# Kernel tuning notes

Hardware: AMD Instinct MI355X
Metric: run time of the kernel (lower is better)

Reference implementation:

```python
import jax, jax.numpy as jnp
import numpy as np

D = 1024      # total input features
R = 32        # number of ragged regions
RMAX = 32     # max region size (padding target)
HIDDEN = [128, 128]
H1, H2 = HIDDEN
B = 8192      # batch size


def _made_masks(r, rmax, hidden):
    """TFP AutoregressiveNetwork masks (left-to-right order, 'equal' hidden degrees,
    params=2, use_bias=False), zero-padded to rmax features."""
    order = np.arange(1, r + 1)
    degs = [order]
    for u in hidden:
        mn = min(int(degs[-1].min()), r - 1)
        degs.append(np.maximum(mn, np.ceil(np.arange(1, u + 1) * (r - 1) / float(u + 1)).astype(np.int64)))
    m1 = np.zeros((rmax, hidden[0]), bool)
    m1[:r] = degs[0][:, None] <= degs[1][None, :]
    m2 = degs[1][:, None] <= degs[2][None, :]
    mout = np.zeros((hidden[-1], rmax * 2), bool)
    out_deg = np.repeat(order, 2)  # output layout is feature-major: [feat, param]
    mout[:, :2 * r] = degs[-1][:, None] < out_deg[None, :]
    return m1, m2, mout


def setup_inputs() -> dict:
    rng = np.random.default_rng(0)
    perm = rng.permutation(D)
    sizes = rng.integers(8, RMAX + 1, size=R)
    idx = np.zeros((R, RMAX), np.int64)
    valid = np.zeros((R, RMAX), bool)
    M1 = np.zeros((R, RMAX, H1), bool)
    M2 = np.zeros((R, H1, H2), bool)
    Mout = np.zeros((R, H2, RMAX * 2), bool)
    pos = 0
    for i in range(R):
        s = int(sizes[i])
        idx[i, :s] = perm[pos:pos + s]
        pos += s
        valid[i, :s] = True
        M1[i], M2[i], Mout[i] = _made_masks(s, RMAX, HIDDEN)
    key = jax.random.key(0)
    k1, k2, k3, k4 = jax.random.split(key, 4)
    inputs = jax.random.normal(k1, (B, D), jnp.float32)
    W1 = jax.random.normal(k2, (R, RMAX, H1), jnp.float32) / np.float32(np.sqrt(RMAX))
    W2 = jax.random.normal(k3, (R, H1, H2), jnp.float32) / np.float32(np.sqrt(H1))
    Wout = jax.random.normal(k4, (R, H2, RMAX * 2), jnp.float32) / np.float32(np.sqrt(H2))
    return {"inputs": inputs, "W1": W1, "W2": W2, "Wout": Wout,
            "idx": jnp.asarray(idx), "valid": jnp.asarray(valid),
            "M1": jnp.asarray(M1), "M2": jnp.asarray(M2), "Mout": jnp.asarray(Mout)}


def reference(inputs, W1, W2, Wout, idx, valid, M1, M2, Mout):
    f = inputs.dtype
    v = valid.astype(f)                              # [R, RMAX]
    xg = jnp.take(inputs, idx, axis=1) * v           # [B, R, RMAX] ragged gather (padded)
    # MADE masked MLP (relu, no bias), batched over all regions at once
    h1 = jax.nn.relu(jnp.einsum('brd,rdh->brh', xg, W1 * M1.astype(f)))
    h2 = jax.nn.relu(jnp.einsum('brh,rhk->brk', h1, W2 * M2.astype(f)))
    out = jnp.einsum('brk,rko->bro', h2, Wout * Mout.astype(f))
    out = out.reshape(out.shape[0], out.shape[1], RMAX, 2)
    shift, log_s = out[..., 0], out[..., 1]
    # MAF inverse: u = (x - shift) * exp(-log_scale); logdet = -sum(log_scale)
    u = (xg - shift) * jnp.exp(-log_s)
    elem = -0.5 * u * u - 0.5 * jnp.log(2.0 * jnp.pi) - log_s
    ll = jnp.sum(elem * v, axis=-1)                  # [B, R]
    return ll[..., None]                             # [B, R, 1] as in tf.stack of expand_dims
```

## Files before the change

kernel.cpp:

```cpp
#include <hip/hip_runtime.h>
#include <math.h>


#define RR 32
#define DD 1024
#define HH 128
#define OO 64
#define TROWS 64
#define TILES 8
#define BLOCKS_PER_R 16

#define SHP 136
#define SXG 40
#define SSC 136

typedef _Float16 f16x8_t __attribute__((ext_vector_type(8)));
typedef float f32x4_t __attribute__((ext_vector_type(4)));
typedef unsigned short u16;
typedef unsigned int u32;

__device__ __forceinline__ u32 pkrtz(float a, float b) {
    union { __fp16 v __attribute__((ext_vector_type(2))); u32 u; } c;
    c.v = __builtin_amdgcn_cvt_pkrtz(a, b);
    return c.u;
}
__device__ __forceinline__ f32x4_t mfma16h(f16x8_t a, f16x8_t b, f32x4_t c) {
    return __builtin_amdgcn_mfma_f32_16x16x32_f16(a, b, c, 0, 0, 0);
}

__device__ __forceinline__ void stage_block16(const float* __restrict__ W,
                                              const int* __restrict__ M,
                                              int ldc, int c0, int K, u16* dst,
                                              int tid)
{
    const int kb = tid >> 3;
    const int cb = tid & 7;
    if (kb * 4 >= K) return;
    const int k0 = kb * 4;
    float e[4][4];
#pragma unroll
    for (int i = 0; i < 4; ++i) {
        const int o = ((k0 + i) * ldc + c0 + 4 * cb) >> 2;
        float4 w = ((const float4*)W)[o];
        int4   m = ((const int4*)M)[o];
        e[i][0] = m.x ? w.x : 0.f; e[i][1] = m.y ? w.y : 0.f;
        e[i][2] = m.z ? w.z : 0.f; e[i][3] = m.w ? w.w : 0.f;
    }
#pragma unroll
    for (int j = 0; j < 4; ++j) {
        uint2 p;
        p.x = pkrtz(e[0][j], e[1][j]);
        p.y = pkrtz(e[2][j], e[3][j]);
        *(uint2*)&dst[(4 * cb + j) * SSC + k0] = p;
    }
}

__device__ __forceinline__ void relu_store16(u16* __restrict__ dst, int o, f32x4_t a)
{
    uint2 s;
    s.x = pkrtz(fmaxf(a[0], 0.f), fmaxf(a[1], 0.f));
    s.y = pkrtz(fmaxf(a[2], 0.f), fmaxf(a[3], 0.f));
    *(uint2*)&dst[o] = s;
}

__global__ __launch_bounds__(512, 4)
void made_flow_r24(const float* __restrict__ inputs,
                   const float* __restrict__ W1,
                   const float* __restrict__ W2,
                   const float* __restrict__ Wout,
                   const int* __restrict__ idx,
                   const int* __restrict__ valid,
                   const int* __restrict__ M1,
                   const int* __restrict__ M2,
                   const int* __restrict__ Mout,
                   float* __restrict__ out)
{
    __shared__ __align__(16) u16 h1s[TROWS * SHP];
    __shared__ __align__(16) u16 h2s[TROWS * SHP];
    __shared__ __align__(16) u16 wout_lds[OO * SSC];
    __shared__ __align__(16) u16 xgh[2][TROWS * SXG];
    __shared__ __align__(16) float red2[2][TROWS][4];
    __shared__ int   idx_s[RR];
    __shared__ float v_s[RR];

    u16* const scr  = h1s;
    u16* const scr2 = h2s;

    const int tid  = threadIdx.x;
    const int r    = blockIdx.x / BLOCKS_PER_R;
    const int rb   = blockIdx.x % BLOCKS_PER_R;
    const int ts64 = rb * TILES * TROWS;

    const int lane = tid & 63;
    const int wave = tid >> 6;
    const int q    = lane >> 4;
    const int l16  = lane & 15;
    const int mq   = wave & 3;
    const int nh   = wave >> 2;
    const int wm3  = wave & 3;
    const int ni3  = wave >> 2;

    if (tid < RR) {
        idx_s[tid] = idx[r * RR + tid];
        v_s[tid]   = valid[r * RR + tid] ? 1.f : 0.f;
    }

    f16x8_t a1[2];
    f16x8_t a2[2][4];
    {
        const float* W1r = W1 + r * RR * HH;   const int* M1r = M1 + r * RR * HH;
        const float* W2r = W2 + r * HH * HH;   const int* M2r = M2 + r * HH * HH;
        const float* Wor = Wout + r * HH * OO; const int* Mor = Mout + r * HH * OO;
        for (int i = 0; i < 2; ++i) {
            __syncthreads();
            if (tid < 256) stage_block16(W2r, M2r, HH, 32 * (2 * i),     HH, scr,  tid);
            else           stage_block16(W2r, M2r, HH, 32 * (2 * i + 1), HH, scr2, tid - 256);
            __syncthreads();
            if (mq == 2 * i) {
#pragma unroll
                for (int mi = 0; mi < 2; ++mi)
#pragma unroll
                    for (int ks = 0; ks < 4; ++ks)
                        a2[mi][ks] = *(const f16x8_t*)&scr[(16 * mi + l16) * SSC + ks * 32 + q * 8];
            } else if (mq == 2 * i + 1) {
#pragma unroll
                for (int mi = 0; mi < 2; ++mi)
#pragma unroll
                    for (int ks = 0; ks < 4; ++ks)
                        a2[mi][ks] = *(const f16x8_t*)&scr2[(16 * mi + l16) * SSC + ks * 32 + q * 8];
            }
        }
        for (int i = 0; i < 2; ++i) {
            __syncthreads();
            if (tid < 256) stage_block16(W1r, M1r, HH, 32 * (2 * i),     RR, scr,  tid);
            else           stage_block16(W1r, M1r, HH, 32 * (2 * i + 1), RR, scr2, tid - 256);
            __syncthreads();
            if (mq == 2 * i) {
#pragma unroll
                for (int mi = 0; mi < 2; ++mi)
                    a1[mi] = *(const f16x8_t*)&scr [(16 * mi + l16) * SSC + q * 8];
            } else if (mq == 2 * i + 1) {
#pragma unroll
                for (int mi = 0; mi < 2; ++mi)
                    a1[mi] = *(const f16x8_t*)&scr2[(16 * mi + l16) * SSC + q * 8];
            }
        }
        if (tid < 256) stage_block16(Wor, Mor, OO, 0,  HH, wout_lds,            tid);
        else           stage_block16(Wor, Mor, OO, 32, HH, wout_lds + 32 * SSC, tid - 256);
    }
    __syncthreads();

    const f32x4_t zero4 = {0.f, 0.f, 0.f, 0.f};
    const int grow = tid >> 4;
    const int gg   = tid & 15;
    const int   ci0 = idx_s[2 * gg], ci1 = idx_s[2 * gg + 1];
    const float cv0 = v_s[2 * gg],   cv1 = v_s[2 * gg + 1];
    const int j0  = 8 * wm3 + 2 * q;
    const float vj0 = v_s[j0], vj1 = v_s[j0 + 1];
    const int gb0 = (ts64 + grow) * DD;
    const int gb1 = (ts64 + 32 + grow) * DD;

    float gx[4];
    {
        float a0 = inputs[gb0 + ci0] * cv0, a1v = inputs[gb0 + ci1] * cv1;
        float b0 = inputs[gb1 + ci0] * cv0, b1v = inputs[gb1 + ci1] * cv1;
        *(u32*)&xgh[0][grow * SXG + 2 * gg]        = pkrtz(a0, a1v);
        *(u32*)&xgh[0][(grow + 32) * SXG + 2 * gg] = pkrtz(b0, b1v);
        gx[0] = inputs[gb0 + TROWS * DD + ci0] * cv0;
        gx[1] = inputs[gb0 + TROWS * DD + ci1] * cv1;
        gx[2] = inputs[gb1 + TROWS * DD + ci0] * cv0;
        gx[3] = inputs[gb1 + TROWS * DD + ci1] * cv1;
    }
    __syncthreads();

    {
#pragma unroll
        for (int nn = 0; nn < 2; ++nn) {
            const int rw = 16 * (2 * nh + nn) + l16;
            f16x8_t b = *(const f16x8_t*)&xgh[0][rw * SXG + q * 8];
#pragma unroll
            for (int mi = 0; mi < 2; ++mi) {
                f32x4_t a = mfma16h(a1[mi], b, zero4);
                relu_store16(h1s, rw * SHP + 32 * mq + 16 * mi + 4 * q, a);
            }
        }
    }

    for (int t = 0; t < TILES; ++t) {
        __syncthreads();

        const bool dg = (t + 1 < TILES);

        if (dg) {
            *(u32*)&xgh[(t + 1) & 1][grow * SXG + 2 * gg]        = pkrtz(gx[0], gx[1]);
            *(u32*)&xgh[(t + 1) & 1][(grow + 32) * SXG + 2 * gg] = pkrtz(gx[2], gx[3]);
        }
        {
            f32x4_t acc[2][2] = {{zero4, zero4}, {zero4, zero4}};
            __builtin_amdgcn_s_setprio(1);
#pragma unroll
            for (int ks = 0; ks < 4; ++ks) {
#pragma unroll
                for (int nn = 0; nn < 2; ++nn) {
                    f16x8_t b = *(const f16x8_t*)&h1s[(16 * (2 * nh + nn) + l16) * SHP + ks * 32 + q * 8];
#pragma unroll
                    for (int mi = 0; mi < 2; ++mi)
                        acc[mi][nn] = mfma16h(a2[mi][ks], b, acc[mi][nn]);
                }
            }
            __builtin_amdgcn_s_setprio(0);
#pragma unroll
            for (int mi = 0; mi < 2; ++mi)
#pragma unroll
                for (int nn = 0; nn < 2; ++nn)
                    relu_store16(h2s, (16 * (2 * nh + nn) + l16) * SHP + 32 * mq + 16 * mi + 4 * q,
                                 acc[mi][nn]);
        }
        if (t >= 2 && tid < TROWS) {
            float4 rv = *(const float4*)&red2[t & 1][tid][0];
            out[((rb * TILES + (t - 2)) * TROWS + tid) * RR + r] =
                rv.x + rv.y + rv.z + rv.w;
        }
        __syncthreads();

        if (t + 2 < TILES) {
            const int base = (t + 2) * (TROWS * DD);
            gx[0] = inputs[gb0 + base + ci0] * cv0;
            gx[1] = inputs[gb0 + base + ci1] * cv1;
            gx[2] = inputs[gb1 + base + ci0] * cv0;
            gx[3] = inputs[gb1 + base + ci1] * cv1;
        }

        f32x4_t acc3[2] = {zero4, zero4};
        __builtin_amdgcn_s_setprio(1);
#pragma unroll
        for (int ks = 0; ks < 4; ++ks) {
            f16x8_t ao = *(const f16x8_t*)&wout_lds[(16 * wm3 + l16) * SSC + ks * 32 + q * 8];
#pragma unroll
            for (int nn = 0; nn < 2; ++nn) {
                f16x8_t b = *(const f16x8_t*)&h2s[(16 * (ni3 + 2 * nn) + l16) * SHP + ks * 32 + q * 8];
                acc3[nn] = mfma16h(ao, b, acc3[nn]);
            }
        }
        __builtin_amdgcn_s_setprio(0);

        if (dg) {
#pragma unroll
            for (int nn = 0; nn < 2; ++nn) {
                const int rw = 16 * (2 * nh + nn) + l16;
                f16x8_t b = *(const f16x8_t*)&xgh[(t + 1) & 1][rw * SXG + q * 8];
#pragma unroll
                for (int mi = 0; mi < 2; ++mi) {
                    f32x4_t a = mfma16h(a1[mi], b, zero4);
                    relu_store16(h1s, rw * SHP + 32 * mq + 16 * mi + 4 * q, a);
                }
            }
        }

#pragma unroll
        for (int nn = 0; nn < 2; ++nn) {
            const int row = 16 * (ni3 + 2 * nn) + l16;
            u32 xw = *(const u32*)&xgh[t & 1][row * SXG + j0];
            union { u32 u; _Float16 h[2]; } xc; xc.u = xw;
            const float xv0 = (float)xc.h[0], xv1 = (float)xc.h[1];
            f32x4_t a = acc3[nn];
            const float u0 = (xv0 - a[0]) * __expf(-a[1]);
            const float u1 = (xv1 - a[2]) * __expf(-a[3]);
            float p = (-0.5f * u0 * u0 - 0.91893853320467266954f - a[1]) * vj0
                    + (-0.5f * u1 * u1 - 0.91893853320467266954f - a[3]) * vj1;
            p += __shfl_xor(p, 16, 64);
            p += __shfl_xor(p, 32, 64);
            if (q == 0) red2[t & 1][row][wm3] = p;
        }
    }

    __syncthreads();
    if (tid < 2 * TROWS) {
        const int tt  = TILES - 2 + (tid >> 6);
        const int row = tid & 63;
        float4 rv = *(const float4*)&red2[tt & 1][row][0];
        out[((rb * TILES + tt) * TROWS + row) * RR + r] =
            rv.x + rv.y + rv.z + rv.w;
    }
}

extern "C" void kernel_launch(void* const* d_in, const int* in_sizes, int n_in,
                              void* d_out, int out_size, void* d_ws, size_t ws_size,
                              hipStream_t stream)
{
    const float* inputs = (const float*)d_in[0];
    const float* W1     = (const float*)d_in[1];
    const float* W2     = (const float*)d_in[2];
    const float* Wout   = (const float*)d_in[3];
    const int*   idx    = (const int*)d_in[4];
    const int*   valid  = (const int*)d_in[5];
    const int*   M1     = (const int*)d_in[6];
    const int*   M2     = (const int*)d_in[7];
    const int*   Mout   = (const int*)d_in[8];
    float*       out    = (float*)d_out;

    hipLaunchKernelGGL(made_flow_r24, dim3(RR * BLOCKS_PER_R), dim3(512), 0, stream,
                       inputs, W1, W2, Wout, idx, valid, M1, M2, Mout, out);
}
```

Before: 117.1 us.

## Halve tile rows and block size, keep Wout fragments in registers

Blocks shrink from 512 to 256 threads with 32-row tiles, and the grid doubles to 32 blocks per region, so each region's rows are spread over more, smaller blocks. Each wave now owns a 32-column slice of every layer, and the Wout fragments are held in registers instead of being reread from a dedicated LDS buffer each tile. This removes the wout_lds array and its per-tile LDS reads and raises block-level parallelism. The cost is that every block redoes the masked-weight staging, so that prologue work doubles overall, and register pressure rises.

```diff
diff --git a/kernel.cpp b/kernel.cpp
--- a/kernel.cpp
+++ b/kernel.cpp
@@ -6,13 +6,14 @@
 #define DD 1024
 #define HH 128
 #define OO 64
-#define TROWS 64
+#define TROWS 32
 #define TILES 8
-#define BLOCKS_PER_R 16
+#define BLOCKS_PER_R 32
 
 #define SHP 136
 #define SXG 40
 #define SSC 136
+#define SW1 40
 
 typedef _Float16 f16x8_t __attribute__((ext_vector_type(8)));
 typedef float f32x4_t __attribute__((ext_vector_type(4)));
@@ -30,8 +31,8 @@
 
 __device__ __forceinline__ void stage_block16(const float* __restrict__ W,
                                               const int* __restrict__ M,
-                                              int ldc, int c0, int K, u16* dst,
-                                              int tid)
+                                              int ldc, int c0, int K,
+                                              u16* dst, int sd, int tid)
 {
     const int kb = tid >> 3;
     const int cb = tid & 7;
@@ -51,7 +52,7 @@
         uint2 p;
         p.x = pkrtz(e[0][j], e[1][j]);
         p.y = pkrtz(e[2][j], e[3][j]);
-        *(uint2*)&dst[(4 * cb + j) * SSC + k0] = p;
+        *(uint2*)&dst[(4 * cb + j) * sd + k0] = p;
     }
 }
 
@@ -63,8 +64,8 @@
     *(uint2*)&dst[o] = s;
 }
 
-__global__ __launch_bounds__(512, 4)
-void made_flow_r24(const float* __restrict__ inputs,
+__global__ __launch_bounds__(256, 4)
+void made_flow_r25(const float* __restrict__ inputs,
                    const float* __restrict__ W1,
                    const float* __restrict__ W2,
                    const float* __restrict__ Wout,
@@ -77,7 +78,6 @@
 {
     __shared__ __align__(16) u16 h1s[TROWS * SHP];
     __shared__ __align__(16) u16 h2s[TROWS * SHP];
-    __shared__ __align__(16) u16 wout_lds[OO * SSC];
     __shared__ __align__(16) u16 xgh[2][TROWS * SXG];
     __shared__ __align__(16) float red2[2][TROWS][4];
     __shared__ int   idx_s[RR];
@@ -89,16 +89,13 @@
     const int tid  = threadIdx.x;
     const int r    = blockIdx.x / BLOCKS_PER_R;
     const int rb   = blockIdx.x % BLOCKS_PER_R;
-    const int ts64 = rb * TILES * TROWS;
+    const int ts   = rb * TILES;
 
     const int lane = tid & 63;
     const int wave = tid >> 6;
     const int q    = lane >> 4;
     const int l16  = lane & 15;
-    const int mq   = wave & 3;
-    const int nh   = wave >> 2;
-    const int wm3  = wave & 3;
-    const int ni3  = wave >> 2;
+    const int mq   = wave;
 
     if (tid < RR) {
         idx_s[tid] = idx[r * RR + tid];
@@ -107,76 +104,81 @@
 
     f16x8_t a1[2];
     f16x8_t a2[2][4];
+    f16x8_t ao[4];
     {
         const float* W1r = W1 + r * RR * HH;   const int* M1r = M1 + r * RR * HH;
         const float* W2r = W2 + r * HH * HH;   const int* M2r = M2 + r * HH * HH;
         const float* Wor = Wout + r * HH * OO; const int* Mor = Mout + r * HH * OO;
-        for (int i = 0; i < 2; ++i) {
+        for (int c = 0; c < 4; ++c) {
             __syncthreads();
-            if (tid < 256) stage_block16(W2r, M2r, HH, 32 * (2 * i),     HH, scr,  tid);
-            else           stage_block16(W2r, M2r, HH, 32 * (2 * i + 1), HH, scr2, tid - 256);
+            stage_block16(W2r, M2r, HH, 32 * c, HH, scr, SSC, tid);
             __syncthreads();
-            if (mq == 2 * i) {
+            if (mq == c) {
 #pragma unroll
                 for (int mi = 0; mi < 2; ++mi)
 #pragma unroll
                     for (int ks = 0; ks < 4; ++ks)
                         a2[mi][ks] = *(const f16x8_t*)&scr[(16 * mi + l16) * SSC + ks * 32 + q * 8];
-            } else if (mq == 2 * i + 1) {
-#pragma unroll
-                for (int mi = 0; mi < 2; ++mi)
-#pragma unroll
-                    for (int ks = 0; ks < 4; ++ks)
-                        a2[mi][ks] = *(const f16x8_t*)&scr2[(16 * mi + l16) * SSC + ks * 32 + q * 8];
-            }
-        }
-        for (int i = 0; i < 2; ++i) {
+            }
+        }
+        for (int c = 0; c < 2; ++c) {
             __syncthreads();
-            if (tid < 256) stage_block16(W1r, M1r, HH, 32 * (2 * i),     RR, scr,  tid);
-            else           stage_block16(W1r, M1r, HH, 32 * (2 * i + 1), RR, scr2, tid - 256);
+            stage_block16(Wor, Mor, OO, 32 * c, HH, scr, SSC, tid);
             __syncthreads();
-            if (mq == 2 * i) {
-#pragma unroll
-                for (int mi = 0; mi < 2; ++mi)
-                    a1[mi] = *(const f16x8_t*)&scr [(16 * mi + l16) * SSC + q * 8];
-            } else if (mq == 2 * i + 1) {
-#pragma unroll
-                for (int mi = 0; mi < 2; ++mi)
-                    a1[mi] = *(const f16x8_t*)&scr2[(16 * mi + l16) * SSC + q * 8];
-            }
-        }
-        if (tid < 256) stage_block16(Wor, Mor, OO, 0,  HH, wout_lds,            tid);
-        else           stage_block16(Wor, Mor, OO, 32, HH, wout_lds + 32 * SSC, tid - 256);
+            if ((wave >> 1) == c) {
+#pragma unroll
+                for (int ks = 0; ks < 4; ++ks)
+                    ao[ks] = *(const f16x8_t*)&scr[(16 * (wave & 1) + l16) * SSC + ks * 32 + q * 8];
+            }
+        }
+        __syncthreads();
+        {
+            const int c  = tid >> 6;
+            const int tp = tid & 63;
+            u16* dst = (c < 2 ? scr : scr2) + 32 * (c & 1) * SW1;
+            stage_block16(W1r, M1r, HH, 32 * c, RR, dst, SW1, tp);
+        }
+        __syncthreads();
+        {
+            const u16* s = (mq < 2) ? scr : scr2;
+#pragma unroll
+            for (int mi = 0; mi < 2; ++mi)
+                a1[mi] = *(const f16x8_t*)&s[(32 * (mq & 1) + 16 * mi + l16) * SW1 + q * 8];
+        }
     }
     __syncthreads();
 
     const f32x4_t zero4 = {0.f, 0.f, 0.f, 0.f};
-    const int grow = tid >> 4;
-    const int gg   = tid & 15;
-    const int   ci0 = idx_s[2 * gg], ci1 = idx_s[2 * gg + 1];
-    const float cv0 = v_s[2 * gg],   cv1 = v_s[2 * gg + 1];
-    const int j0  = 8 * wm3 + 2 * q;
+    const int grow = tid >> 3;
+    const int gg   = tid & 7;
+    int   ci[4]; float cv[4];
+#pragma unroll
+    for (int u = 0; u < 4; ++u) {
+        ci[u] = idx_s[4 * gg + u];
+        cv[u] = v_s[4 * gg + u];
+    }
+    const int j0  = 8 * mq + 2 * q;
     const float vj0 = v_s[j0], vj1 = v_s[j0 + 1];
-    const int gb0 = (ts64 + grow) * DD;
-    const int gb1 = (ts64 + 32 + grow) * DD;
+    const int gbase = (ts * TROWS + grow) * DD;
 
     float gx[4];
     {
-        float a0 = inputs[gb0 + ci0] * cv0, a1v = inputs[gb0 + ci1] * cv1;
-        float b0 = inputs[gb1 + ci0] * cv0, b1v = inputs[gb1 + ci1] * cv1;
-        *(u32*)&xgh[0][grow * SXG + 2 * gg]        = pkrtz(a0, a1v);
-        *(u32*)&xgh[0][(grow + 32) * SXG + 2 * gg] = pkrtz(b0, b1v);
-        gx[0] = inputs[gb0 + TROWS * DD + ci0] * cv0;
-        gx[1] = inputs[gb0 + TROWS * DD + ci1] * cv1;
-        gx[2] = inputs[gb1 + TROWS * DD + ci0] * cv0;
-        gx[3] = inputs[gb1 + TROWS * DD + ci1] * cv1;
+        float a0 = inputs[gbase + ci[0]] * cv[0];
+        float a1v = inputs[gbase + ci[1]] * cv[1];
+        float a2v = inputs[gbase + ci[2]] * cv[2];
+        float a3 = inputs[gbase + ci[3]] * cv[3];
+        uint2 p; p.x = pkrtz(a0, a1v); p.y = pkrtz(a2v, a3);
+        *(uint2*)&xgh[0][grow * SXG + 4 * gg] = p;
+#pragma unroll
+        for (int u = 0; u < 4; ++u)
+            gx[u] = inputs[gbase + TROWS * DD + ci[u]] * cv[u];
     }
     __syncthreads();
 
     {
 #pragma unroll
-        for (int nn = 0; nn < 2; ++nn) {
-            const int rw = 16 * (2 * nh + nn) + l16;
+        for (int ni = 0; ni < 2; ++ni) {
+            const int rw = 16 * ni + l16;
             f16x8_t b = *(const f16x8_t*)&xgh[0][rw * SXG + q * 8];
 #pragma unroll
             for (int mi = 0; mi < 2; ++mi) {
@@ -192,8 +194,8 @@
         const bool dg = (t + 1 < TILES);
 
         if (dg) {
-            *(u32*)&xgh[(t + 1) & 1][grow * SXG + 2 * gg]        = pkrtz(gx[0], gx[1]);
-            *(u32*)&xgh[(t + 1) & 1][(grow + 32) * SXG + 2 * gg] = pkrtz(gx[2], gx[3]);
+            uint2 p; p.x = pkrtz(gx[0], gx[1]); p.y = pkrtz(gx[2], gx[3]);
+            *(uint2*)&xgh[(t + 1) & 1][grow * SXG + 4 * gg] = p;
         }
         {
             f32x4_t acc[2][2] = {{zero4, zero4}, {zero4, zero4}};
@@ -201,53 +203,51 @@
 #pragma unroll
             for (int ks = 0; ks < 4; ++ks) {
 #pragma unroll
-                for (int nn = 0; nn < 2; ++nn) {
-                    f16x8_t b = *(const f16x8_t*)&h1s[(16 * (2 * nh + nn) + l16) * SHP + ks * 32 + q * 8];
+                for (int ni = 0; ni < 2; ++ni) {
+                    f16x8_t b = *(const f16x8_t*)&h1s[(16 * ni + l16) * SHP + ks * 32 + q * 8];
 #pragma unroll
                     for (int mi = 0; mi < 2; ++mi)
-                        acc[mi][nn] = mfma16h(a2[mi][ks], b, acc[mi][nn]);
+                        acc[mi][ni] = mfma16h(a2[mi][ks], b, acc[mi][ni]);
                 }
             }
             __builtin_amdgcn_s_setprio(0);
 #pragma unroll
             for (int mi = 0; mi < 2; ++mi)
 #pragma unroll
-                for (int nn = 0; nn < 2; ++nn)
-                    relu_store16(h2s, (16 * (2 * nh + nn) + l16) * SHP + 32 * mq + 16 * mi + 4 * q,
-                                 acc[mi][nn]);
+                for (int ni = 0; ni < 2; ++ni)
+                    relu_store16(h2s, (16 * ni + l16) * SHP + 32 * mq + 16 * mi + 4 * q,
+                                 acc[mi][ni]);
         }
         if (t >= 2 && tid < TROWS) {
             float4 rv = *(const float4*)&red2[t & 1][tid][0];
-            out[((rb * TILES + (t - 2)) * TROWS + tid) * RR + r] =
+            out[((ts + (t - 2)) * TROWS + tid) * RR + r] =
                 rv.x + rv.y + rv.z + rv.w;
         }
         __syncthreads();
 
         if (t + 2 < TILES) {
-            const int base = (t + 2) * (TROWS * DD);
-            gx[0] = inputs[gb0 + base + ci0] * cv0;
-            gx[1] = inputs[gb0 + base + ci1] * cv1;
-            gx[2] = inputs[gb1 + base + ci0] * cv0;
-            gx[3] = inputs[gb1 + base + ci1] * cv1;
+            const int base = gbase + (t + 2) * (TROWS * DD);
+#pragma unroll
+            for (int u = 0; u < 4; ++u)
+                gx[u] = inputs[base + ci[u]] * cv[u];
         }
 
         f32x4_t acc3[2] = {zero4, zero4};
         __builtin_amdgcn_s_setprio(1);
 #pragma unroll
         for (int ks = 0; ks < 4; ++ks) {
-            f16x8_t ao = *(const f16x8_t*)&wout_lds[(16 * wm3 + l16) * SSC + ks * 32 + q * 8];
-#pragma unroll
-            for (int nn = 0; nn < 2; ++nn) {
-                f16x8_t b = *(const f16x8_t*)&h2s[(16 * (ni3 + 2 * nn) + l16) * SHP + ks * 32 + q * 8];
-                acc3[nn] = mfma16h(ao, b, acc3[nn]);
+#pragma unroll
+            for (int ni = 0; ni < 2; ++ni) {
+                f16x8_t b = *(const f16x8_t*)&h2s[(16 * ni + l16) * SHP + ks * 32 + q * 8];
+                acc3[ni] = mfma16h(ao[ks], b, acc3[ni]);
             }
         }
         __builtin_amdgcn_s_setprio(0);
 
         if (dg) {
 #pragma unroll
-            for (int nn = 0; nn < 2; ++nn) {
-                const int rw = 16 * (2 * nh + nn) + l16;
+            for (int ni = 0; ni < 2; ++ni) {
+                const int rw = 16 * ni + l16;
                 f16x8_t b = *(const f16x8_t*)&xgh[(t + 1) & 1][rw * SXG + q * 8];
 #pragma unroll
                 for (int mi = 0; mi < 2; ++mi) {
@@ -258,28 +258,28 @@
         }
 
 #pragma unroll
-        for (int nn = 0; nn < 2; ++nn) {
-            const int row = 16 * (ni3 + 2 * nn) + l16;
+        for (int ni = 0; ni < 2; ++ni) {
+            const int row = 16 * ni + l16;
             u32 xw = *(const u32*)&xgh[t & 1][row * SXG + j0];
             union { u32 u; _Float16 h[2]; } xc; xc.u = xw;
             const float xv0 = (float)xc.h[0], xv1 = (float)xc.h[1];
-            f32x4_t a = acc3[nn];
+            f32x4_t a = acc3[ni];
             const float u0 = (xv0 - a[0]) * __expf(-a[1]);
             const float u1 = (xv1 - a[2]) * __expf(-a[3]);
             float p = (-0.5f * u0 * u0 - 0.91893853320467266954f - a[1]) * vj0
                     + (-0.5f * u1 * u1 - 0.91893853320467266954f - a[3]) * vj1;
             p += __shfl_xor(p, 16, 64);
             p += __shfl_xor(p, 32, 64);
-            if (q == 0) red2[t & 1][row][wm3] = p;
+            if (q == 0) red2[t & 1][row][mq] = p;
         }
     }
 
     __syncthreads();
     if (tid < 2 * TROWS) {
-        const int tt  = TILES - 2 + (tid >> 6);
-        const int row = tid & 63;
+        const int tt  = TILES - 2 + (tid >> 5);
+        const int row = tid & 31;
         float4 rv = *(const float4*)&red2[tt & 1][row][0];
-        out[((rb * TILES + tt) * TROWS + row) * RR + r] =
+        out[((ts + tt) * TROWS + row) * RR + r] =
             rv.x + rv.y + rv.z + rv.w;
     }
 }
@@ -299,6 +299,6 @@
     const int*   Mout   = (const int*)d_in[8];
     float*       out    = (float*)d_out;
 
-    hipLaunchKernelGGL(made_flow_r24, dim3(RR * BLOCKS_PER_R), dim3(512), 0, stream,
+    hipLaunchKernelGGL(made_flow_r25, dim3(RR * BLOCKS_PER_R), dim3(256), 0, stream,
                        inputs, W1, W2, Wout, idx, valid, M1, M2, Mout, out);
 }
```

Measured after the change: 121.8 us. 1.04x slower.
